# Kernel tuning notes

Measured on AMD Instinct MI355X. Metric: run time of the kernel, lower is better.

The kernel has to match this reference:

```python
import jax, jax.numpy as jnp
import numpy as np

E = 64      # n_routed_experts
T = 32768   # total routed tokens
K = 1024    # hidden_size
I = 512     # moe_intermediate_size
C = 1024


def setup_inputs() -> dict:
    key = jax.random.key(0)
    k1, k2, k3 = jax.random.split(key, 3)
    x = jax.random.normal(k1, (T, K), dtype=jnp.float32)
    # uniform routing: 512 tokens per expert, sums to T
    tokens_per_expert = jnp.full((E,), T // E, dtype=jnp.int32)
    w13 = jax.random.normal(k2, (E, K, 2 * I), dtype=jnp.float32) * 0.02  # fused w1/w3
    w2 = jax.random.normal(k3, (E, I, K), dtype=jnp.float32) * 0.02
    return {"x": x, "tokens_per_expert": tokens_per_expert, "w13": w13, "w2": w2, "decoding": 0}


def reference(x, tokens_per_expert, w13, w2, decoding):
    # Tokens are laid out contiguously by expert (grouped-GEMM convention).
    starts = jnp.cumsum(tokens_per_expert) - tokens_per_expert           # [E]
    eid = jnp.repeat(jnp.arange(E), tokens_per_expert, total_repeat_length=T)  # [T]
    pos = jnp.arange(T) - starts[eid]                                    # slot within expert
    # dispatch to dense [E, C, K] buffer (zero-padded beyond each expert's count)
    xb = jnp.zeros((E, C, K), x.dtype).at[eid, pos].set(x)
    # grouped GEMM 1: fused w1w3  -> [E, C, 2I]
    gate_up = jnp.einsum('eck,ekn->ecn', xb, w13)
    # SwiGLU: split last dim into gate / up
    gate, up = jnp.split(gate_up, 2, axis=-1)
    h = jax.nn.silu(gate) * up                                           # [E, C, I]
    # grouped GEMM 2: fused w2 -> [E, C, K]
    yb = jnp.einsum('eci,eik->eck', h, w2)
    # gather back to token order [T, K]
    return yb[eid, pos]
```

## Files before the change

### kernel.cpp

```cpp
#include <hip/hip_runtime.h>
#include <hip/hip_bf16.h>
#include <stdint.h>

#define NEXP 64
#define TTOK 32768
#define HID  1024
#define IMID 512
#define CAP  1024

typedef __bf16 bf16x8 __attribute__((ext_vector_type(8)));
typedef float  f32x4  __attribute__((ext_vector_type(4)));

static __device__ __forceinline__ unsigned int f2bf_u(float f) {
    __hip_bfloat16 h = __float2bfloat16(f);
    return (unsigned int)*reinterpret_cast<unsigned short*>(&h);
}
static __device__ __forceinline__ unsigned int pack2(float lo, float hi) {
    return f2bf_u(lo) | (f2bf_u(hi) << 16);
}
static __device__ __forceinline__ unsigned short f2bf_s(float f) {
    __hip_bfloat16 h = __float2bfloat16(f);
    return *reinterpret_cast<unsigned short*>(&h);
}

static __device__ __forceinline__ void gload16(const void* g, void* l) {
    __builtin_amdgcn_global_load_lds(
        (const __attribute__((address_space(1))) unsigned int*)g,
        (__attribute__((address_space(3))) unsigned int*)l,
        16, 0, 0);
}

static __device__ __forceinline__ int expert_start(const int* tpe, int e, int lane) {
    int v = tpe[lane];
    int contrib = (lane < e) ? v : 0;
    #pragma unroll
    for (int off = 1; off < 64; off <<= 1)
        contrib += __shfl_xor(contrib, off, 64);
    return contrib;
}


static __device__ __forceinline__ void w13_tile_cvt(const float* __restrict__ w13,
                                                    unsigned short* __restrict__ w13p,
                                                    int e, int k0, int n0, int t, char* lds) {
    unsigned short (*Tl)[72] = reinterpret_cast<unsigned short(*)[72]>(lds);
    const int kl = t >> 4, nl = (t & 15) * 4;
    const float* src = w13 + ((size_t)e << 20) + (size_t)k0 * 1024 + n0;
    #pragma unroll
    for (int p = 0; p < 4; ++p) {
        int k = kl + p * 16;
        f32x4 v = *reinterpret_cast<const f32x4*>(src + (size_t)k * 1024 + nl);
        uint2 wv; wv.x = pack2(v.x, v.y); wv.y = pack2(v.z, v.w);
        *reinterpret_cast<uint2*>(&Tl[k][nl]) = wv;
    }
    __syncthreads();
    const int nloc = t >> 2, kc = (t & 3) * 16;
    const int n = n0 + nloc;
    const int icol = n & 511, isup = n >> 9;
    const int np = (icol >> 5) * 64 + isup * 32 + (icol & 31);
    unsigned int v32[8];
    #pragma unroll
    for (int j = 0; j < 8; ++j)
        v32[j] = (unsigned int)Tl[kc + 2 * j][nloc] |
                 ((unsigned int)Tl[kc + 2 * j + 1][nloc] << 16);
    unsigned short* dst = w13p + ((size_t)e << 20) + (size_t)np * 1024 + k0 + kc;
    uint4 o0 = {v32[0], v32[1], v32[2], v32[3]};
    uint4 o1 = {v32[4], v32[5], v32[6], v32[7]};
    *reinterpret_cast<uint4*>(dst)     = o0;
    *reinterpret_cast<uint4*>(dst + 8) = o1;
}

static __device__ __forceinline__ void w2_tile_cvt(const float* __restrict__ w2,
                                                   unsigned short* __restrict__ w2p,
                                                   int tile, int t, char* lds) {
    const int e  = tile >> 7;
    const int k0 = ((tile >> 4) & 7) * 64;
    const int n0 = (tile & 15) * 64;
    unsigned short (*Tl)[72] = reinterpret_cast<unsigned short(*)[72]>(lds);
    const int kl = t >> 4, nl = (t & 15) * 4;
    const float* src = w2 + (size_t)e * (IMID * HID) + (size_t)k0 * 1024 + n0;
    #pragma unroll
    for (int p = 0; p < 4; ++p) {
        int k = kl + p * 16;
        f32x4 v = *reinterpret_cast<const f32x4*>(src + (size_t)k * 1024 + nl);
        uint2 wv; wv.x = pack2(v.x, v.y); wv.y = pack2(v.z, v.w);
        *reinterpret_cast<uint2*>(&Tl[k][nl]) = wv;
    }
    __syncthreads();
    const int nloc = t >> 2, kc = (t & 3) * 16;
    unsigned int v32[8];
    #pragma unroll
    for (int j = 0; j < 8; ++j)
        v32[j] = (unsigned int)Tl[kc + 2 * j][nloc] |
                 ((unsigned int)Tl[kc + 2 * j + 1][nloc] << 16);
    unsigned short* dst = w2p + (size_t)e * (HID * IMID) + (size_t)(n0 + nloc) * IMID + k0 + kc;
    uint4 o0 = {v32[0], v32[1], v32[2], v32[3]};
    uint4 o1 = {v32[4], v32[5], v32[6], v32[7]};
    *reinterpret_cast<uint4*>(dst)     = o0;
    *reinterpret_cast<uint4*>(dst + 8) = o1;
}

static __device__ __forceinline__ void gemm1_body(
    const unsigned short* __restrict__ xbf, const int* __restrict__ tpe,
    const unsigned short* __restrict__ w13p, unsigned short* __restrict__ hbuf,
    int ebase, int bid, int t, char* lds) {
    const int work = (bid & 7) * 128 + (bid >> 3);
    const int e  = ebase + (work >> 5);
    const int nt = (work >> 3) & 3;
    const int mt = work & 7;
    const int lane = t & 63, w = t >> 6;

    int cnt = tpe[e]; if (cnt > CAP) cnt = CAP;
    const int m0 = mt * 128;
    if (m0 >= cnt) return;
    const int start = expert_start(tpe, e, lane);

    char* As = lds;
    char* Bs = lds + 16384;
    const int wr = w >> 1, wc = w & 1;
    const int r = lane & 15, q = lane >> 4;

    f32x4 acc[4][8];
    const f32x4 z4 = {0.f, 0.f, 0.f, 0.f};
    #pragma unroll
    for (int i = 0; i < 4; ++i)
        #pragma unroll
        for (int j = 0; j < 8; ++j) acc[i][j] = z4;

    const int swb = ((lane & 7) ^ (lane >> 3)) << 4;
    const char* aP = (const char*)xbf;
    const char* bP = (const char*)w13p + ((size_t)e << 21) + ((size_t)nt << 19);

    for (int kt = 0; kt < 16; ++kt) {
        __syncthreads();
        const int kb = kt * 128;
        #pragma unroll
        for (int i = 0; i < 4; ++i) {
            const int srow = w * 32 + i * 8 + (lane >> 3);
            long ar = (long)start + m0 + srow;
            if (ar > TTOK - 1) ar = TTOK - 1;
            gload16(aP + ar * 2048 + kb + swb, As + w * 4096 + i * 1024);
        }
        #pragma unroll
        for (int i = 0; i < 8; ++i) {
            const int srow = w * 64 + i * 8 + (lane >> 3);
            gload16(bP + (size_t)srow * 2048 + kb + swb, Bs + w * 8192 + i * 1024);
        }
        __syncthreads();
        #pragma unroll
        for (int kk = 0; kk < 2; ++kk) {
            bf16x8 af[4], bf[8];
            #pragma unroll
            for (int fm = 0; fm < 4; ++fm) {
                int row = (wr << 6) + (fm << 4) + r;
                af[fm] = *reinterpret_cast<const bf16x8*>(
                    As + row * 128 + ((kk * 64 + q * 16) ^ ((row & 7) << 4)));
            }
            #pragma unroll
            for (int fn = 0; fn < 8; ++fn) {
                int row = (wc << 7) + (fn << 4) + r;
                bf[fn] = *reinterpret_cast<const bf16x8*>(
                    Bs + row * 128 + ((kk * 64 + q * 16) ^ ((row & 7) << 4)));
            }
            #pragma unroll
            for (int fm = 0; fm < 4; ++fm)
                #pragma unroll
                for (int fn = 0; fn < 8; ++fn)
                    acc[fm][fn] = __builtin_amdgcn_mfma_f32_16x16x32_bf16(
                        af[fm], bf[fn], acc[fm][fn], 0, 0, 0);
        }
    }

    #pragma unroll
    for (int fm = 0; fm < 4; ++fm) {
        int mb = m0 + (wr << 6) + (fm << 4) + (q << 2);
        #pragma unroll
        for (int c2 = 0; c2 < 2; ++c2) {
            #pragma unroll
            for (int fp = 0; fp < 2; ++fp) {
                f32x4 g = acc[fm][c2 * 4 + fp];
                f32x4 u = acc[fm][c2 * 4 + 2 + fp];
                int icol = (nt * 4 + wc * 2 + c2) * 32 + fp * 16 + r;
                #pragma unroll
                for (int v = 0; v < 4; ++v) {
                    if (mb + v < cnt) {
                        float gv = g[v];
                        float sv = (gv / (1.f + __expf(-gv))) * u[v];
                        hbuf[(size_t)(start + mb + v) * IMID + icol] = f2bf_s(sv);
                    }
                }
            }
        }
    }
}

__global__ __launch_bounds__(256)
void phase1(const float* __restrict__ x, unsigned short* __restrict__ xbf,
            const float* __restrict__ w13, unsigned short* __restrict__ w13p) {
    __shared__ alignas(16) char lds[9216];
    const int bid = blockIdx.x;
    const int t   = threadIdx.x;
    if (bid < 16384) {
        size_t i = ((size_t)bid * 256 + t) * 8;
        f32x4 a = *reinterpret_cast<const f32x4*>(x + i);
        f32x4 b = *reinterpret_cast<const f32x4*>(x + i + 4);
        uint4 o;
        o.x = pack2(a.x, a.y); o.y = pack2(a.z, a.w);
        o.z = pack2(b.x, b.y); o.w = pack2(b.z, b.w);
        *reinterpret_cast<uint4*>(xbf + i) = o;
    } else {
        const int tile = bid - 16384;
        const int e  = tile >> 8;
        const int k0 = ((tile >> 4) & 15) * 64;
        const int n0 = (tile & 15) * 64;
        w13_tile_cvt(w13, w13p, e, k0, n0, t, lds);
    }
}

__global__ __launch_bounds__(256, 2)
void phase2(const unsigned short* __restrict__ xbf, const int* __restrict__ tpe,
            const unsigned short* __restrict__ w13p, unsigned short* __restrict__ hbuf,
            const float* __restrict__ w13) {
    __shared__ alignas(16) char lds[49152];
    const int bid = blockIdx.x;
    const int t   = threadIdx.x;
    if (bid < 1024) {
        gemm1_body(xbf, tpe, w13p, hbuf, 0, bid, t, lds);
    } else {
        const int tile = bid - 1024;
        const int e  = 32 + (tile >> 8);
        const int k0 = ((tile >> 4) & 15) * 64;
        const int n0 = (tile & 15) * 64;
        w13_tile_cvt(w13, (unsigned short*)w13p, e, k0, n0, t, lds);
    }
}

__global__ __launch_bounds__(256, 2)
void phase3(const unsigned short* __restrict__ xbf, const int* __restrict__ tpe,
            const unsigned short* __restrict__ w13p, unsigned short* __restrict__ hbuf,
            const float* __restrict__ w2, unsigned short* __restrict__ w2p) {
    __shared__ alignas(16) char lds[49152];
    const int bid = blockIdx.x;
    const int t   = threadIdx.x;
    if (bid < 1024) {
        gemm1_body(xbf, tpe, w13p, hbuf, 32, bid, t, lds);
    } else {
        w2_tile_cvt(w2, w2p, bid - 1024, t, lds);
    }
}

__global__ __launch_bounds__(256, 2)
void gemm2(const unsigned short* __restrict__ hbuf,
           const int* __restrict__ tpe,
           const unsigned short* __restrict__ w2p,
           float* __restrict__ out) {
    __shared__ alignas(16) char lds[49152];
    const int bid  = blockIdx.x;
    const int work = (bid & 7) * 256 + (bid >> 3);
    const int e  = work >> 5;
    const int nt = (work >> 3) & 3;
    const int mt = work & 7;

    const int t = threadIdx.x, lane = t & 63, w = t >> 6;
    int cnt = tpe[e]; if (cnt > CAP) cnt = CAP;
    const int m0 = mt * 128;
    if (m0 >= cnt) return;
    const int start = expert_start(tpe, e, lane);

    char* As = lds;
    char* Bs = lds + 16384;
    const int wr = w >> 1, wc = w & 1;
    const int r = lane & 15, q = lane >> 4;

    f32x4 acc[4][8];
    const f32x4 z4 = {0.f, 0.f, 0.f, 0.f};
    #pragma unroll
    for (int i = 0; i < 4; ++i)
        #pragma unroll
        for (int j = 0; j < 8; ++j) acc[i][j] = z4;

    const int swb = ((lane & 7) ^ (lane >> 3)) << 4;
    const char* aP = (const char*)hbuf;
    const char* bP = (const char*)w2p + ((size_t)e << 20) + ((size_t)nt << 18);

    for (int kt = 0; kt < 8; ++kt) {
        __syncthreads();
        const int kb = kt * 128;
        #pragma unroll
        for (int i = 0; i < 4; ++i) {
            const int srow = w * 32 + i * 8 + (lane >> 3);
            long ar = (long)start + m0 + srow;
            if (ar > TTOK - 1) ar = TTOK - 1;
            gload16(aP + ar * 1024 + kb + swb, As + w * 4096 + i * 1024);
        }
        #pragma unroll
        for (int i = 0; i < 8; ++i) {
            const int srow = w * 64 + i * 8 + (lane >> 3);
            gload16(bP + (size_t)srow * 1024 + kb + swb, Bs + w * 8192 + i * 1024);
        }
        __syncthreads();
        #pragma unroll
        for (int kk = 0; kk < 2; ++kk) {
            bf16x8 af[4], bf[8];
            #pragma unroll
            for (int fm = 0; fm < 4; ++fm) {
                int row = (wr << 6) + (fm << 4) + r;
                af[fm] = *reinterpret_cast<const bf16x8*>(
                    As + row * 128 + ((kk * 64 + q * 16) ^ ((row & 7) << 4)));
            }
            #pragma unroll
            for (int fn = 0; fn < 8; ++fn) {
                int row = (wc << 7) + (fn << 4) + r;
                bf[fn] = *reinterpret_cast<const bf16x8*>(
                    Bs + row * 128 + ((kk * 64 + q * 16) ^ ((row & 7) << 4)));
            }
            #pragma unroll
            for (int fm = 0; fm < 4; ++fm)
                #pragma unroll
                for (int fn = 0; fn < 8; ++fn)
                    acc[fm][fn] = __builtin_amdgcn_mfma_f32_16x16x32_bf16(
                        af[fm], bf[fn], acc[fm][fn], 0, 0, 0);
        }
    }

    #pragma unroll
    for (int fm = 0; fm < 4; ++fm) {
        int mb = m0 + (wr << 6) + (fm << 4) + (q << 2);
        #pragma unroll
        for (int fn = 0; fn < 8; ++fn) {
            int ocol = (nt << 8) + (wc << 7) + (fn << 4) + r;
            #pragma unroll
            for (int v = 0; v < 4; ++v) {
                if (mb + v < cnt)
                    out[(size_t)(start + mb + v) * HID + ocol] = acc[fm][fn][v];
            }
        }
    }
}

extern "C" void kernel_launch(void* const* d_in, const int* in_sizes, int n_in,
                              void* d_out, int out_size, void* d_ws, size_t ws_size,
                              hipStream_t stream) {
    const float* x   = (const float*)d_in[0];
    const int*   tpe = (const int*)d_in[1];
    const float* w13 = (const float*)d_in[2];
    const float* w2  = (const float*)d_in[3];
    float* out = (float*)d_out;

    char* ws = (char*)d_ws;
    unsigned short* xbf  = (unsigned short*)(ws);
    unsigned short* hbuf = (unsigned short*)(ws + 67108864);
    unsigned short* w13p = (unsigned short*)(ws + 67108864 + 33554432);
    unsigned short* w2p  = (unsigned short*)(ws + 67108864 + 33554432 + 134217728);

    phase1<<<dim3(24576, 1, 1), dim3(256, 1, 1), 0, stream>>>(x, xbf, w13, w13p);
    phase2<<<dim3(9216, 1, 1), dim3(256, 1, 1), 0, stream>>>(xbf, tpe, w13p, hbuf, w13);
    phase3<<<dim3(9216, 1, 1), dim3(256, 1, 1), 0, stream>>>(xbf, tpe, w13p, hbuf, w2, w2p);
    gemm2 <<<dim3(2048, 1, 1), dim3(256, 1, 1), 0, stream>>>(hbuf, tpe, w2p, out);
}
```

Baseline: 285.4 us.

## Fuse x fp32-to-bf16 conversion into GEMM1 A-tile loading with register prefetch

Drops the separate pass that turns x into a bf16 staging buffer. GEMM1 now reads fp32 x directly, converts it in registers and writes the swizzled A tile to LDS, prefetching the next k-tile's A into registers while the MFMAs run. This removes a 128MB read plus 64MB write round trip and shrinks phase1. In exchange each GEMM1 block reads x at fp32 width, and x is re-read once per N-tile (four times per expert half), which raises register pressure and global traffic inside the GEMM.

```diff
diff --git a/kernel.cpp b/kernel.cpp
--- a/kernel.cpp
+++ b/kernel.cpp
@@ -101,7 +101,7 @@
 }
 
 static __device__ __forceinline__ void gemm1_body(
-    const unsigned short* __restrict__ xbf, const int* __restrict__ tpe,
+    const float* __restrict__ x, const int* __restrict__ tpe,
     const unsigned short* __restrict__ w13p, unsigned short* __restrict__ hbuf,
     int ebase, int bid, int t, char* lds) {
     const int work = (bid & 7) * 128 + (bid >> 3);
@@ -128,25 +128,51 @@
         for (int j = 0; j < 8; ++j) acc[i][j] = z4;
 
     const int swb = ((lane & 7) ^ (lane >> 3)) << 4;
-    const char* aP = (const char*)xbf;
     const char* bP = (const char*)w13p + ((size_t)e << 21) + ((size_t)nt << 19);
 
+    const int arow = t >> 3;
+    const int akc  = t & 7;
+    long arows[4];
+    #pragma unroll
+    for (int p = 0; p < 4; ++p) {
+        long ar = (long)start + m0 + p * 32 + arow;
+        if (ar > TTOK - 1) ar = TTOK - 1;
+        arows[p] = ar;
+    }
+
+    f32x4 pa[8];
+    #define LOADA(kt_)                                                          \
+        _Pragma("unroll")                                                       \
+        for (int p = 0; p < 4; ++p) {                                           \
+            const float* sp = x + arows[p] * 1024 + (kt_) * 64 + akc * 8;       \
+            pa[2 * p]     = *reinterpret_cast<const f32x4*>(sp);                \
+            pa[2 * p + 1] = *reinterpret_cast<const f32x4*>(sp + 4);            \
+        }
+    #define WRITEA()                                                            \
+        _Pragma("unroll")                                                       \
+        for (int p = 0; p < 4; ++p) {                                           \
+            int rr = p * 32 + arow;                                             \
+            uint4 o;                                                            \
+            o.x = pack2(pa[2 * p].x,     pa[2 * p].y);                          \
+            o.y = pack2(pa[2 * p].z,     pa[2 * p].w);                          \
+            o.z = pack2(pa[2 * p + 1].x, pa[2 * p + 1].y);                      \
+            o.w = pack2(pa[2 * p + 1].z, pa[2 * p + 1].w);                      \
+            *reinterpret_cast<uint4*>(As + rr * 128 +                           \
+                ((akc * 16) ^ ((rr & 7) << 4))) = o;                            \
+        }
+
+    LOADA(0);
     for (int kt = 0; kt < 16; ++kt) {
         __syncthreads();
         const int kb = kt * 128;
         #pragma unroll
-        for (int i = 0; i < 4; ++i) {
-            const int srow = w * 32 + i * 8 + (lane >> 3);
-            long ar = (long)start + m0 + srow;
-            if (ar > TTOK - 1) ar = TTOK - 1;
-            gload16(aP + ar * 2048 + kb + swb, As + w * 4096 + i * 1024);
-        }
-        #pragma unroll
         for (int i = 0; i < 8; ++i) {
             const int srow = w * 64 + i * 8 + (lane >> 3);
             gload16(bP + (size_t)srow * 2048 + kb + swb, Bs + w * 8192 + i * 1024);
         }
+        WRITEA();
         __syncthreads();
+        if (kt < 15) { LOADA(kt + 1); }
         #pragma unroll
         for (int kk = 0; kk < 2; ++kk) {
             bf16x8 af[4], bf[8];
@@ -170,6 +196,8 @@
                         af[fm], bf[fn], acc[fm][fn], 0, 0, 0);
         }
     }
+    #undef LOADA
+    #undef WRITEA
 
     #pragma unroll
     for (int fm = 0; fm < 4; ++fm) {
@@ -195,37 +223,25 @@
 }
 
 __global__ __launch_bounds__(256)
-void phase1(const float* __restrict__ x, unsigned short* __restrict__ xbf,
-            const float* __restrict__ w13, unsigned short* __restrict__ w13p) {
+void phase1(const float* __restrict__ w13, unsigned short* __restrict__ w13p) {
     __shared__ alignas(16) char lds[9216];
     const int bid = blockIdx.x;
     const int t   = threadIdx.x;
-    if (bid < 16384) {
-        size_t i = ((size_t)bid * 256 + t) * 8;
-        f32x4 a = *reinterpret_cast<const f32x4*>(x + i);
-        f32x4 b = *reinterpret_cast<const f32x4*>(x + i + 4);
-        uint4 o;
-        o.x = pack2(a.x, a.y); o.y = pack2(a.z, a.w);
-        o.z = pack2(b.x, b.y); o.w = pack2(b.z, b.w);
-        *reinterpret_cast<uint4*>(xbf + i) = o;
-    } else {
-        const int tile = bid - 16384;
-        const int e  = tile >> 8;
-        const int k0 = ((tile >> 4) & 15) * 64;
-        const int n0 = (tile & 15) * 64;
-        w13_tile_cvt(w13, w13p, e, k0, n0, t, lds);
-    }
+    const int e  = bid >> 8;
+    const int k0 = ((bid >> 4) & 15) * 64;
+    const int n0 = (bid & 15) * 64;
+    w13_tile_cvt(w13, w13p, e, k0, n0, t, lds);
 }
 
 __global__ __launch_bounds__(256, 2)
-void phase2(const unsigned short* __restrict__ xbf, const int* __restrict__ tpe,
+void phase2(const float* __restrict__ x, const int* __restrict__ tpe,
             const unsigned short* __restrict__ w13p, unsigned short* __restrict__ hbuf,
             const float* __restrict__ w13) {
     __shared__ alignas(16) char lds[49152];
     const int bid = blockIdx.x;
     const int t   = threadIdx.x;
     if (bid < 1024) {
-        gemm1_body(xbf, tpe, w13p, hbuf, 0, bid, t, lds);
+        gemm1_body(x, tpe, w13p, hbuf, 0, bid, t, lds);
     } else {
         const int tile = bid - 1024;
         const int e  = 32 + (tile >> 8);
@@ -236,14 +252,14 @@
 }
 
 __global__ __launch_bounds__(256, 2)
-void phase3(const unsigned short* __restrict__ xbf, const int* __restrict__ tpe,
+void phase3(const float* __restrict__ x, const int* __restrict__ tpe,
             const unsigned short* __restrict__ w13p, unsigned short* __restrict__ hbuf,
             const float* __restrict__ w2, unsigned short* __restrict__ w2p) {
     __shared__ alignas(16) char lds[49152];
     const int bid = blockIdx.x;
     const int t   = threadIdx.x;
     if (bid < 1024) {
-        gemm1_body(xbf, tpe, w13p, hbuf, 32, bid, t, lds);
+        gemm1_body(x, tpe, w13p, hbuf, 32, bid, t, lds);
     } else {
         w2_tile_cvt(w2, w2p, bid - 1024, t, lds);
     }
@@ -348,13 +364,12 @@
     float* out = (float*)d_out;
 
     char* ws = (char*)d_ws;
-    unsigned short* xbf  = (unsigned short*)(ws);
-    unsigned short* hbuf = (unsigned short*)(ws + 67108864);
-    unsigned short* w13p = (unsigned short*)(ws + 67108864 + 33554432);
-    unsigned short* w2p  = (unsigned short*)(ws + 67108864 + 33554432 + 134217728);
-
-    phase1<<<dim3(24576, 1, 1), dim3(256, 1, 1), 0, stream>>>(x, xbf, w13, w13p);
-    phase2<<<dim3(9216, 1, 1), dim3(256, 1, 1), 0, stream>>>(xbf, tpe, w13p, hbuf, w13);
-    phase3<<<dim3(9216, 1, 1), dim3(256, 1, 1), 0, stream>>>(xbf, tpe, w13p, hbuf, w2, w2p);
+    unsigned short* hbuf = (unsigned short*)(ws);
+    unsigned short* w13p = (unsigned short*)(ws + 33554432);
+    unsigned short* w2p  = (unsigned short*)(ws + 33554432 + 134217728);
+
+    phase1<<<dim3(8192, 1, 1), dim3(256, 1, 1), 0, stream>>>(w13, w13p);
+    phase2<<<dim3(9216, 1, 1), dim3(256, 1, 1), 0, stream>>>(x, tpe, w13p, hbuf, w13);
+    phase3<<<dim3(9216, 1, 1), dim3(256, 1, 1), 0, stream>>>(x, tpe, w13p, hbuf, w2, w2p);
     gemm2 <<<dim3(2048, 1, 1), dim3(256, 1, 1), 0, stream>>>(hbuf, tpe, w2p, out);
 }
```

Result: no change. 282.9 us (-0.9%).
